# Optimization experiments

Measured on AMD Instinct MI355X. Metric: run time of the kernel, lower is better.

## Reference

```python
import jax, jax.numpy as jnp
import numpy as np

D_ENC, D_DEC, HID = 512, 512, 256

def setup_inputs() -> dict:
    key = jax.random.key(0)
    ks = jax.random.split(key, 8)
    B, T, U = 4, 800, 150
    enc = jax.random.normal(ks[0], (B, T, D_ENC), dtype=jnp.float32)
    dec = jax.random.normal(ks[1], (B, U, D_DEC), dtype=jnp.float32)
    s_e = 1.0 / np.sqrt(D_ENC)
    s_d = 1.0 / np.sqrt(D_DEC)
    s_h = 1.0 / np.sqrt(HID)
    W_enc = jax.random.uniform(ks[2], (D_ENC, HID), jnp.float32, -s_e, s_e)
    b_enc = jax.random.uniform(ks[3], (HID,), jnp.float32, -s_e, s_e)
    W_dec = jax.random.uniform(ks[4], (D_DEC, HID), jnp.float32, -s_d, s_d)
    b_dec = jax.random.uniform(ks[5], (HID,), jnp.float32, -s_d, s_d)
    w_score = jax.random.uniform(ks[6], (HID,), jnp.float32, -s_h, s_h)
    b_score = jax.random.uniform(ks[7], (), jnp.float32, -s_h, s_h)
    return {"encoder_out": enc, "decoder_out": dec,
            "W_enc": W_enc, "b_enc": b_enc,
            "W_dec": W_dec, "b_dec": b_dec,
            "w_score": w_score, "b_score": b_score}

def reference(encoder_out, decoder_out, W_enc, b_enc, W_dec, b_dec, w_score, b_score):
    # enc_proj: [B,T,H], dec_proj: [B,U,H]
    enc_proj = jnp.einsum('bte,eh->bth', encoder_out, W_enc) + b_enc
    dec_proj = jnp.einsum('bud,dh->buh', decoder_out, W_dec) + b_dec
    # Broadcast-add + tanh -> [B,T,U,H], then reduce H with score vector.
    combined = jnp.tanh(enc_proj[:, :, None, :] + dec_proj[:, None, :, :])
    score = jnp.einsum('btuh,h->btu', combined, w_score) + b_score
    # Softmax over decoder tokens (last dim U).
    return jax.nn.softmax(score, axis=-1)
```

## Files before the change

kernel.cpp:

```cpp
#include <hip/hip_runtime.h>
#include <hip/hip_bf16.h>

#define B_ 4
#define T_ 800
#define U_ 150
#define D_ 512
#define H_ 256
#define PADH2 132

static constexpr float ARG_SCALE = 2.8853900817779268f;
static constexpr float LOG2E_F   = 1.4426950408889634f;

typedef __attribute__((ext_vector_type(8))) short bf16x8;
typedef __attribute__((ext_vector_type(4))) float f32x4;

extern "C" __device__ float __ocml_exp2_f32(float);

__device__ __forceinline__ float fast_exp2(float x) {
#if __has_builtin(__builtin_amdgcn_exp2f)
    return __builtin_amdgcn_exp2f(x);
#else
    return __ocml_exp2_f32(x);
#endif
}
__device__ __forceinline__ float fast_rcp(float x) {
#if __has_builtin(__builtin_amdgcn_rcpf)
    return __builtin_amdgcn_rcpf(x);
#else
    return 1.0f / x;
#endif
}

__device__ __forceinline__ void bf16split(float x, unsigned short& hi, unsigned short& lo) {
    unsigned u = __builtin_bit_cast(unsigned, x);
    unsigned r = (u + 0x7FFFu + ((u >> 16) & 1u)) >> 16;
    hi = (unsigned short)r;
    float fh = __builtin_bit_cast(float, r << 16);
    float d = x - fh;
    unsigned u2 = __builtin_bit_cast(unsigned, d);
    unsigned r2 = (u2 + 0x7FFFu + ((u2 >> 16) & 1u)) >> 16;
    lo = (unsigned short)r2;
}

__global__ __launch_bounds__(256) void conv_kernel(
    const float* __restrict__ enc, const float* __restrict__ dec,
    const float* __restrict__ W_enc, const float* __restrict__ W_dec,
    unsigned short* __restrict__ WtEh, unsigned short* __restrict__ WtEl,
    unsigned short* __restrict__ WtDh, unsigned short* __restrict__ WtDl,
    unsigned short* __restrict__ AEh, unsigned short* __restrict__ AEl,
    unsigned short* __restrict__ ADh, unsigned short* __restrict__ ADl)
{
    const int nthreads = 952 * 256;
    const int gtid = blockIdx.x * 256 + threadIdx.x;

    for (int i = gtid; i < 2 * D_ * H_; i += nthreads) {
        const int which = i >> 17;
        const int r = i & (D_ * H_ - 1);
        const int e = r >> 8, h = r & 255;
        const float x = ARG_SCALE * (which ? W_dec[r] : W_enc[r]);
        unsigned short hi, lo; bf16split(x, hi, lo);
        const int s = e >> 5, q = (e >> 3) & 3, j = e & 7;
        const int g = h >> 4, rr = h & 15, l = q * 16 + rr;
        const size_t idx = (size_t)(s * 16 + g) * 512 + l * 8 + j;
        if (which) { WtDh[idx] = hi; WtDl[idx] = lo; }
        else       { WtEh[idx] = hi; WtEl[idx] = lo; }
    }

    {
        const int u = gtid;
        const int c = u >> 10;
        const int rem = u & 1023;
        const int s = rem >> 6, l = rem & 63;
        const float* in; unsigned short *oh, *ol; int cl, rmax;
        if (c < 200) { in = enc; oh = AEh; ol = AEl; cl = c;       rmax = 3199; }
        else         { in = dec; oh = ADh; ol = ADl; cl = c - 200; rmax = 599; }
        int row = cl * 16 + (l & 15); if (row > rmax) row = rmax;
        const int e0 = s * 32 + (l >> 4) * 8;
        const float4 f0 = ((const float4*)(in + (size_t)row * D_ + e0))[0];
        const float4 f1 = ((const float4*)(in + (size_t)row * D_ + e0))[1];
        const float v[8] = {f0.x, f0.y, f0.z, f0.w, f1.x, f1.y, f1.z, f1.w};
        bf16x8 ah, al;
        #pragma unroll
        for (int j = 0; j < 8; ++j) {
            unsigned short hi, lo; bf16split(v[j], hi, lo);
            ah[j] = (short)hi; al[j] = (short)lo;
        }
        const size_t di = ((size_t)(cl * 16 + s) * 64 + l) * 8;
        *(bf16x8*)&oh[di] = ah;
        *(bf16x8*)&ol[di] = al;
    }
}

__global__ __launch_bounds__(256) void proj_mfma_kernel(
    const unsigned short* __restrict__ WtEh, const unsigned short* __restrict__ WtEl,
    const unsigned short* __restrict__ WtDh, const unsigned short* __restrict__ WtDl,
    const unsigned short* __restrict__ AEh, const unsigned short* __restrict__ AEl,
    const unsigned short* __restrict__ ADh, const unsigned short* __restrict__ ADl,
    const float* __restrict__ b_enc, const float* __restrict__ b_dec,
    float* __restrict__ Ee, float* __restrict__ Ed)
{
    const int tid = threadIdx.x;
    int blk = blockIdx.x;
    const unsigned short *Ah_, *Al_, *Wh_, *Wl_; const float* bias;
    float* outp; int rmax;
    if (blk < 800) { Ah_ = AEh; Al_ = AEl; Wh_ = WtEh; Wl_ = WtEl;
                     bias = b_enc; outp = Ee; rmax = 3199; }
    else { blk -= 800; Ah_ = ADh; Al_ = ADl; Wh_ = WtDh; Wl_ = WtDl;
           bias = b_dec; outp = Ed; rmax = 599; }
    const int cl = blk >> 2, hq = blk & 3;
    const int row0 = cl * 16;

    const int lane = tid & 63, w = tid >> 6;
    const int q = lane >> 4, r15 = lane & 15;
    const int g = 4 * hq + w;

    const unsigned short* ap_h = Ah_ + ((size_t)(cl * 16) * 64 + lane) * 8;
    const unsigned short* ap_l = Al_ + ((size_t)(cl * 16) * 64 + lane) * 8;
    const unsigned short* bp_h = Wh_ + (size_t)g * 512 + lane * 8;
    const unsigned short* bp_l = Wl_ + (size_t)g * 512 + lane * 8;

    f32x4 acc = {0.f, 0.f, 0.f, 0.f};
    #pragma unroll 4
    for (int s = 0; s < 16; ++s) {
        const bf16x8 ah = *(const bf16x8*)(ap_h + (size_t)s * 512);
        const bf16x8 al = *(const bf16x8*)(ap_l + (size_t)s * 512);
        const bf16x8 bh = *(const bf16x8*)(bp_h + (size_t)s * 8192);
        const bf16x8 bl = *(const bf16x8*)(bp_l + (size_t)s * 8192);
        acc = __builtin_amdgcn_mfma_f32_16x16x32_bf16(ah, bh, acc, 0, 0, 0);
        acc = __builtin_amdgcn_mfma_f32_16x16x32_bf16(ah, bl, acc, 0, 0, 0);
        acc = __builtin_amdgcn_mfma_f32_16x16x32_bf16(al, bh, acc, 0, 0, 0);
    }

    const int h = g * 16 + r15;
    const float bv = bias[h];
    #pragma unroll
    for (int reg = 0; reg < 4; ++reg) {
        const int trow = row0 + 4 * q + reg;
        if (trow <= rmax)
            outp[(size_t)trow * H_ + h] = fast_exp2(fmaf(ARG_SCALE, bv, acc[reg]));
    }
}

__global__ __launch_bounds__(128) void score_kernel(
    const float* __restrict__ Ee, const float* __restrict__ Ed,
    const float* __restrict__ w_score,
    float* __restrict__ sc0, float* __restrict__ sc1)
{
    const int tid = threadIdx.x;
    const int ut = blockIdx.x % 5, hs = blockIdx.x / 5;
    const int tt = blockIdx.y, b = blockIdx.z;

    __shared__ float eld[32][PADH2];
    __shared__ float dld[32][PADH2];

    const int t0 = tt * 32, u0 = ut * 32;
    const int hoff = hs * 128;

    #pragma unroll
    for (int k = 0; k < 8; ++k) {
        int idx = tid + 128 * k;
        int row = idx >> 5;
        int f4  = idx & 31;
        *(float4*)&eld[row][4 * f4] =
            *(const float4*)(Ee + (size_t)(b * T_ + t0 + row) * H_ + hoff + 4 * f4);
        int du = u0 + row; if (du > U_ - 1) du = U_ - 1;
        *(float4*)&dld[row][4 * f4] =
            *(const float4*)(Ed + (size_t)(b * U_ + du) * H_ + hoff + 4 * f4);
    }
    __syncthreads();

    const int tx = tid & 15, ty = tid >> 4;
    const float* e0 = &eld[4 * ty + 0][0];
    const float* e1 = &eld[4 * ty + 1][0];
    const float* e2 = &eld[4 * ty + 2][0];
    const float* e3 = &eld[4 * ty + 3][0];
    const float* d0 = &dld[tx][0];
    const float* d1 = &dld[tx + 16][0];
    const float* wp = w_score + hoff;

    float a00 = 0.f, a01 = 0.f, a10 = 0.f, a11 = 0.f;
    float a20 = 0.f, a21 = 0.f, a30 = 0.f, a31 = 0.f;

#define SQUAD(EV, DV, A) { \
    float q0 = fmaf(EV.x, DV.x, 1.f); \
    float q1 = fmaf(EV.y, DV.y, 1.f); \
    float q2 = fmaf(EV.z, DV.z, 1.f); \
    float q3 = fmaf(EV.w, DV.w, 1.f); \
    float Dab = q0 * q1, Dcd = q2 * q3; \
    float Nab = fmaf(w.x, q1, w.y * q0); \
    float Ncd = fmaf(w.z, q3, w.w * q2); \
    float N = fmaf(Nab, Dcd, Ncd * Dab); \
    A = fmaf(N, fast_rcp(Dab * Dcd), A); }

    #pragma unroll 4
    for (int h4 = 0; h4 < 32; ++h4) {
        const float4 w  = ((const float4*)wp)[h4];
        const float4 ea = *(const float4*)(e0 + 4 * h4);
        const float4 eb = *(const float4*)(e1 + 4 * h4);
        const float4 ec = *(const float4*)(e2 + 4 * h4);
        const float4 ed = *(const float4*)(e3 + 4 * h4);
        const float4 da = *(const float4*)(d0 + 4 * h4);
        const float4 db = *(const float4*)(d1 + 4 * h4);
        SQUAD(ea, da, a00) SQUAD(ea, db, a01)
        SQUAD(eb, da, a10) SQUAD(eb, db, a11)
        SQUAD(ec, da, a20) SQUAD(ec, db, a21)
        SQUAD(ed, da, a30) SQUAD(ed, db, a31)
    }
#undef SQUAD

    const float s0[4] = {a00, a10, a20, a30};
    const float s1[4] = {a01, a11, a21, a31};

    float* sout = hs ? sc1 : sc0;
    const int ua = u0 + tx, ub = ua + 16;
    #pragma unroll
    for (int j = 0; j < 4; ++j) {
        const int t = t0 + 4 * ty + j;
        const size_t base = (size_t)(b * T_ + t) * U_;
        sout[base + ua] = s0[j];
        if (ub < U_) sout[base + ub] = s1[j];
    }
}

__global__ __launch_bounds__(256) void softmax_kernel(
    const float* __restrict__ sc0, const float* __restrict__ sc1,
    float* __restrict__ out)
{
    const int tid  = threadIdx.x;
    const int wave = tid >> 6, lane = tid & 63;
    const int row  = blockIdx.x * 4 + wave;
    const size_t base = (size_t)row * U_;

    float z0 = -2.f * (sc0[base + lane]      + sc1[base + lane]);
    float z1 = -2.f * (sc0[base + lane + 64] + sc1[base + lane + 64]);
    const bool v2 = (lane + 128) < U_;
    float z2 = v2 ? -2.f * (sc0[base + lane + 128] + sc1[base + lane + 128])
                  : -INFINITY;

    float m = fmaxf(fmaxf(z0, z1), z2);
    #pragma unroll
    for (int off = 32; off > 0; off >>= 1) m = fmaxf(m, __shfl_xor(m, off));

    float p0 = fast_exp2((z0 - m) * LOG2E_F);
    float p1 = fast_exp2((z1 - m) * LOG2E_F);
    float p2 = v2 ? fast_exp2((z2 - m) * LOG2E_F) : 0.f;

    float s = p0 + p1 + p2;
    #pragma unroll
    for (int off = 32; off > 0; off >>= 1) s += __shfl_xor(s, off);

    const float inv = 1.0f / s;
    out[base + lane]      = p0 * inv;
    out[base + lane + 64] = p1 * inv;
    if (v2) out[base + lane + 128] = p2 * inv;
}

extern "C" void kernel_launch(void* const* d_in, const int* in_sizes, int n_in,
                              void* d_out, int out_size, void* d_ws, size_t ws_size,
                              hipStream_t stream) {
    const float* enc     = (const float*)d_in[0];
    const float* dec     = (const float*)d_in[1];
    const float* W_enc   = (const float*)d_in[2];
    const float* b_enc   = (const float*)d_in[3];
    const float* W_dec   = (const float*)d_in[4];
    const float* b_dec   = (const float*)d_in[5];
    const float* w_score = (const float*)d_in[6];

    float* ws  = (float*)d_ws;
    float* Ee  = ws;
    float* Ed  = Ee + 819200;
    float* sc0 = Ed + 153600;
    float* sc1 = sc0 + 480000;
    unsigned short* WtEh = (unsigned short*)(sc1 + 480000);
    unsigned short* WtEl = WtEh + 131072;
    unsigned short* WtDh = WtEl + 131072;
    unsigned short* WtDl = WtDh + 131072;
    unsigned short* AEh  = WtDl + 131072;
    unsigned short* AEl  = AEh + 1638400;
    unsigned short* ADh  = AEl + 1638400;
    unsigned short* ADl  = ADh + 311296;
    float* out = (float*)d_out;

    conv_kernel<<<952, 256, 0, stream>>>(enc, dec, W_enc, W_dec,
                                         WtEh, WtEl, WtDh, WtDl,
                                         AEh, AEl, ADh, ADl);
    proj_mfma_kernel<<<952, 256, 0, stream>>>(WtEh, WtEl, WtDh, WtDl,
                                              AEh, AEl, ADh, ADl,
                                              b_enc, b_dec, Ee, Ed);
    score_kernel<<<dim3(10, 25, 4), 128, 0, stream>>>(Ee, Ed, w_score, sc0, sc1);
    softmax_kernel<<<800, 256, 0, stream>>>(sc0, sc1, out);
}
```

Baseline: 42.00 us.

## Enlarge score kernel register tile to 4x4 with 64-row encoder tile

```diff
diff --git a/kernel.cpp b/kernel.cpp
--- a/kernel.cpp
+++ b/kernel.cpp
@@ -6,7 +6,7 @@
 #define U_ 150
 #define D_ 512
 #define H_ 256
-#define PADH2 132
+#define SLDS 130
 
 static constexpr float ARG_SCALE = 2.8853900817779268f;
 static constexpr float LOG2E_F   = 1.4426950408889634f;
@@ -150,36 +150,40 @@
     const int ut = blockIdx.x % 5, hs = blockIdx.x / 5;
     const int tt = blockIdx.y, b = blockIdx.z;
 
-    __shared__ float eld[32][PADH2];
-    __shared__ float dld[32][PADH2];
-
-    const int t0 = tt * 32, u0 = ut * 32;
+    __shared__ float eld[64][SLDS];
+    __shared__ float dld[32][SLDS];
+
+    const int t0 = tt * 64, u0 = ut * 32;
     const int hoff = hs * 128;
 
     #pragma unroll
+    for (int k = 0; k < 16; ++k) {
+        const int idx = tid + 128 * k;
+        const int row = idx >> 5, f4 = idx & 31;
+        int tr = t0 + row; if (tr > T_ - 1) tr = T_ - 1;
+        *(float4*)&eld[row][4 * f4] =
+            *(const float4*)(Ee + (size_t)(b * T_ + tr) * H_ + hoff + 4 * f4);
+    }
+    #pragma unroll
     for (int k = 0; k < 8; ++k) {
-        int idx = tid + 128 * k;
-        int row = idx >> 5;
-        int f4  = idx & 31;
-        *(float4*)&eld[row][4 * f4] =
-            *(const float4*)(Ee + (size_t)(b * T_ + t0 + row) * H_ + hoff + 4 * f4);
+        const int idx = tid + 128 * k;
+        const int row = idx >> 5, f4 = idx & 31;
         int du = u0 + row; if (du > U_ - 1) du = U_ - 1;
         *(float4*)&dld[row][4 * f4] =
             *(const float4*)(Ed + (size_t)(b * U_ + du) * H_ + hoff + 4 * f4);
     }
     __syncthreads();
 
-    const int tx = tid & 15, ty = tid >> 4;
-    const float* e0 = &eld[4 * ty + 0][0];
-    const float* e1 = &eld[4 * ty + 1][0];
-    const float* e2 = &eld[4 * ty + 2][0];
-    const float* e3 = &eld[4 * ty + 3][0];
-    const float* d0 = &dld[tx][0];
-    const float* d1 = &dld[tx + 16][0];
+    const int tx = tid & 7, ty = tid >> 3;
+    const float* ep = &eld[4 * ty][0];
+    const float* dp = &dld[tx][0];
     const float* wp = w_score + hoff;
 
-    float a00 = 0.f, a01 = 0.f, a10 = 0.f, a11 = 0.f;
-    float a20 = 0.f, a21 = 0.f, a30 = 0.f, a31 = 0.f;
+    float acc[4][4];
+    #pragma unroll
+    for (int j = 0; j < 4; ++j)
+        #pragma unroll
+        for (int k = 0; k < 4; ++k) acc[j][k] = 0.f;
 
 #define SQUAD(EV, DV, A) { \
     float q0 = fmaf(EV.x, DV.x, 1.f); \
@@ -192,33 +196,36 @@
     float N = fmaf(Nab, Dcd, Ncd * Dab); \
     A = fmaf(N, fast_rcp(Dab * Dcd), A); }
 
-    #pragma unroll 4
+    #pragma unroll 2
     for (int h4 = 0; h4 < 32; ++h4) {
-        const float4 w  = ((const float4*)wp)[h4];
-        const float4 ea = *(const float4*)(e0 + 4 * h4);
-        const float4 eb = *(const float4*)(e1 + 4 * h4);
-        const float4 ec = *(const float4*)(e2 + 4 * h4);
-        const float4 ed = *(const float4*)(e3 + 4 * h4);
-        const float4 da = *(const float4*)(d0 + 4 * h4);
-        const float4 db = *(const float4*)(d1 + 4 * h4);
-        SQUAD(ea, da, a00) SQUAD(ea, db, a01)
-        SQUAD(eb, da, a10) SQUAD(eb, db, a11)
-        SQUAD(ec, da, a20) SQUAD(ec, db, a21)
-        SQUAD(ed, da, a30) SQUAD(ed, db, a31)
+        const float4 w = ((const float4*)wp)[h4];
+        float4 ev[4], dv[4];
+        #pragma unroll
+        for (int j = 0; j < 4; ++j)
+            ev[j] = *(const float4*)(ep + (size_t)j * SLDS + 4 * h4);
+        #pragma unroll
+        for (int k = 0; k < 4; ++k)
+            dv[k] = *(const float4*)(dp + (size_t)(8 * k) * SLDS + 4 * h4);
+        #pragma unroll
+        for (int j = 0; j < 4; ++j)
+            #pragma unroll
+            for (int k = 0; k < 4; ++k)
+                SQUAD(ev[j], dv[k], acc[j][k])
     }
 #undef SQUAD
 
-    const float s0[4] = {a00, a10, a20, a30};
-    const float s1[4] = {a01, a11, a21, a31};
-
     float* sout = hs ? sc1 : sc0;
-    const int ua = u0 + tx, ub = ua + 16;
     #pragma unroll
     for (int j = 0; j < 4; ++j) {
         const int t = t0 + 4 * ty + j;
-        const size_t base = (size_t)(b * T_ + t) * U_;
-        sout[base + ua] = s0[j];
-        if (ub < U_) sout[base + ub] = s1[j];
+        if (t < T_) {
+            const size_t base = (size_t)(b * T_ + t) * U_;
+            #pragma unroll
+            for (int k = 0; k < 4; ++k) {
+                const int u = u0 + tx + 8 * k;
+                if (u < U_) sout[base + u] = acc[j][k];
+            }
+        }
     }
 }
 
@@ -287,6 +294,6 @@
     proj_mfma_kernel<<<952, 256, 0, stream>>>(WtEh, WtEl, WtDh, WtDl,
                                               AEh, AEl, ADh, ADl,
                                               b_enc, b_dec, Ee, Ed);
-    score_kernel<<<dim3(10, 25, 4), 128, 0, stream>>>(Ee, Ed, w_score, sc0, sc1);
+    score_kernel<<<dim3(10, 13, 4), 128, 0, stream>>>(Ee, Ed, w_score, sc0, sc1);
     softmax_kernel<<<800, 256, 0, stream>>>(sc0, sc1, out);
 }
```

Measured after the change: 64.19 us. +52.9%, slower.
